# Kernel optimization log

Hardware: AMD Instinct MI355X
Metric: run time of the kernel (lower is better)

Reference implementation:

```python
import jax, jax.numpy as jnp
import numpy as np
from jax import lax

B, S, H, I, E, TOP_K = 4, 4096, 2048, 1024, 8, 2


def setup_inputs() -> dict:
    key = jax.random.key(0)
    k1, k2, k3, k4, k5 = jax.random.split(key, 5)
    scale = 0.02  # realistic init scale so router logits are well-conditioned
    return {
        "x": jax.random.normal(k1, (B, S, H), dtype=jnp.float32),
        "gate_w": jax.random.normal(k2, (E, H), dtype=jnp.float32) * scale,
        "wg": jax.random.normal(k3, (E, H, I), dtype=jnp.float32) * scale,
        "wu": jax.random.normal(k4, (E, H, I), dtype=jnp.float32) * scale,
        "wd": jax.random.normal(k5, (E, I, H), dtype=jnp.float32) * scale,
    }


def reference(x, gate_w, wg, wu, wd):
    b, s, h = x.shape
    xt = x.reshape(b * s, h)                      # [T, H]
    router_logits = xt @ gate_w.T                 # [T, E]
    probs = jax.nn.softmax(router_logits, axis=-1)
    topk_w, topk_idx = lax.top_k(probs, TOP_K)    # [T, K]
    T = xt.shape[0]
    # combine[t, e] = routing weight of expert e for token t (0 if not in top-k)
    combine = jnp.zeros((T, E), xt.dtype).at[
        jnp.arange(T)[:, None], topk_idx
    ].set(topk_w)

    # scan over experts; each step is one grouped SwiGLU MLP over all tokens,
    # weighted by the (mostly-zero) combine column -> identical math to the
    # torch gather/index_add dispatch.
    def step(acc, ew):
        wgi, wui, wdi, c = ew                     # [H,I],[H,I],[I,H],[T]
        hdn = jax.nn.silu(xt @ wgi) * (xt @ wui)  # [T, I]
        return acc + c[:, None] * (hdn @ wdi), None

    acc, _ = lax.scan(step, jnp.zeros_like(xt), (wg, wu, wd, combine.T))
    return acc.reshape(b, s, h), router_logits
```

## Files before the change

kernel.cpp:

```cpp
#include <hip/hip_runtime.h>

#define T_TOK 16384
#define H_DIM 2048
#define I_DIM 1024
#define E_NUM 8

static const size_t F_WGT = 0;
static const size_t F_WUT = 33554432ull;
static const size_t F_XH  = 67108864ull;
static const size_t F_Y2  = 0;
static const size_t F_WDT = 134217728ull;
static const size_t F_HDN = 167772160ull;
static const size_t F_TOK = 234881024ull;
static const size_t F_WT  = 235405312ull;
static const size_t F_IDX = 235929600ull;
static const size_t F_CNT = 236060672ull;

typedef float f32x4 __attribute__((ext_vector_type(4)));
typedef _Float16 f16x8 __attribute__((ext_vector_type(8)));
typedef _Float16 f16x4 __attribute__((ext_vector_type(4)));

__device__ __forceinline__ void gload_lds16(const void* g, void* l) {
  __builtin_amdgcn_global_load_lds(
      (const __attribute__((address_space(1))) unsigned int*)g,
      (__attribute__((address_space(3))) unsigned int*)l, 16, 0, 0);
}

__global__ __launch_bounds__(256) void wconv_kernel(
    const float* __restrict__ wg, const float* __restrict__ wu,
    const float* __restrict__ wd, _Float16* __restrict__ wgT,
    _Float16* __restrict__ wuT, _Float16* __restrict__ wdT) {
  const int bx = blockIdx.x;
  const int w = bx >> 12;
  const int r2 = bx & 4095;
  const int e = r2 >> 9;
  const int t = r2 & 511;

  const float* src;
  _Float16* dst;
  int R, C;
  if (w == 0)      { src = wg; dst = wgT; R = H_DIM; C = I_DIM; }
  else if (w == 1) { src = wu; dst = wuT; R = H_DIM; C = I_DIM; }
  else             { src = wd; dst = wdT; R = I_DIM; C = H_DIM; }
  src += (size_t)e * R * C;
  dst += (size_t)e * R * C;

  const int tiles_c = C >> 6;
  const int tr = t / tiles_c;
  const int tc = t % tiles_c;

  __shared__ float tile[64][65];
  const int tid = threadIdx.x;

#pragma unroll
  for (int c = 0; c < 4; ++c) {
    const int q = c * 256 + tid;
    const int row = q >> 4;
    const int col4 = (q & 15) * 4;
    const float4 v = *(const float4*)(src + (size_t)(tr * 64 + row) * C + tc * 64 + col4);
    tile[row][col4 + 0] = v.x;
    tile[row][col4 + 1] = v.y;
    tile[row][col4 + 2] = v.z;
    tile[row][col4 + 3] = v.w;
  }
  __syncthreads();
#pragma unroll
  for (int c = 0; c < 4; ++c) {
    const int q = c * 256 + tid;
    const int row = q >> 4;
    const int col4 = (q & 15) * 4;
    f16x4 o = { (_Float16)tile[col4 + 0][row], (_Float16)tile[col4 + 1][row],
                (_Float16)tile[col4 + 2][row], (_Float16)tile[col4 + 3][row] };
    *(f16x4*)(dst + (size_t)(tc * 64 + row) * R + tr * 64 + col4) = o;
  }
}

__global__ __launch_bounds__(256) void router_kernel(
    const float* __restrict__ x, const float* __restrict__ gw,
    float* __restrict__ logits, int* __restrict__ tok_list,
    float* __restrict__ wt_list, int* __restrict__ idx2,
    int* __restrict__ counts, _Float16* __restrict__ xh) {
  const int lane = threadIdx.x & 63;
  const int wave = threadIdx.x >> 6;
  const int t = blockIdx.x * 4 + wave;
  const float* xr = x + (size_t)t * H_DIM;

  float xv[32];
#pragma unroll
  for (int j = 0; j < 32; ++j) xv[j] = xr[lane + j * 64];

  _Float16* xhr = xh + (size_t)t * H_DIM;
#pragma unroll
  for (int j = 0; j < 32; ++j) xhr[lane + j * 64] = (_Float16)xv[j];

  float lg[E_NUM];
#pragma unroll
  for (int e = 0; e < E_NUM; ++e) {
    const float* gr = gw + e * H_DIM;
    float s = 0.f;
#pragma unroll
    for (int j = 0; j < 32; ++j) s += xv[j] * gr[lane + j * 64];
#pragma unroll
    for (int off = 32; off > 0; off >>= 1) s += __shfl_xor(s, off, 64);
    lg[e] = s;
  }

  if (lane == 0) {
#pragma unroll
    for (int e = 0; e < E_NUM; ++e) logits[(size_t)t * E_NUM + e] = lg[e];
    float mx = lg[0];
#pragma unroll
    for (int e = 1; e < E_NUM; ++e) mx = fmaxf(mx, lg[e]);
    float se = 0.f;
#pragma unroll
    for (int e = 0; e < E_NUM; ++e) se += expf(lg[e] - mx);
    int i1 = 0; float b1 = lg[0];
#pragma unroll
    for (int e = 1; e < E_NUM; ++e) { if (lg[e] > b1) { b1 = lg[e]; i1 = e; } }
    int i2 = -1; float b2 = -1e30f;
#pragma unroll
    for (int e = 0; e < E_NUM; ++e) { if (e != i1 && lg[e] > b2) { b2 = lg[e]; i2 = e; } }
    const float p1 = expf(b1 - mx) / se;
    const float p2 = expf(b2 - mx) / se;
    int pos = atomicAdd(&counts[i1], 1);
    tok_list[i1 * T_TOK + pos] = t;
    wt_list[i1 * T_TOK + pos] = p1;
    idx2[t * 2] = (i1 << 16) | pos;
    pos = atomicAdd(&counts[i2], 1);
    tok_list[i2 * T_TOK + pos] = t;
    wt_list[i2 * T_TOK + pos] = p2;
    idx2[t * 2 + 1] = (i2 << 16) | pos;
  }
}

__global__ __launch_bounds__(256) void gemm1_kernel(
    const _Float16* __restrict__ xh, const _Float16* __restrict__ wgT,
    const _Float16* __restrict__ wuT, const int* __restrict__ tok_list,
    const int* __restrict__ counts, _Float16* __restrict__ hdn) {
  const int cpx = (E_NUM * 128 * 8) >> 3;
  int bx = blockIdx.x;
  bx = (bx & 7) * cpx + (bx >> 3);

  const int cb = bx & 7;
  const int rb = (bx >> 3) & 127;
  const int e = bx >> 10;
  const int n_e = counts[e];
  const int row0 = rb * 128;
  if (row0 >= n_e) return;
  int goff = 0;
#pragma unroll
  for (int j = 0; j < E_NUM; ++j) goff += (j < e) ? counts[j] : 0;
  const int rem = min(128, n_e - row0);

  __shared__ int toks[128];
  __shared__ __attribute__((aligned(16))) _Float16 As[2][128 * 32];
  __shared__ __attribute__((aligned(16))) _Float16 Bg[2][128 * 32];
  __shared__ __attribute__((aligned(16))) _Float16 Bu[2][128 * 32];

  const int tid = threadIdx.x;
  if (tid < 128) {
    int idx = row0 + tid;
    if (idx > n_e - 1) idx = n_e - 1;
    toks[tid] = tok_list[e * T_TOK + idx];
  }
  __syncthreads();

  const int lane = tid & 63;
  const int wid = tid >> 6;
  const int wr = (wid >> 1) * 64;
  const int wcl = (wid & 1) * 64;
  const int n0 = cb * 128;

  const _Float16* wgTe = wgT + ((size_t)e * I_DIM + n0) * H_DIM;
  const _Float16* wuTe = wuT + ((size_t)e * I_DIM + n0) * H_DIM;

  const _Float16* asrc[2];
  int bofs[2], dofs[2];
#pragma unroll
  for (int c = 0; c < 2; ++c) {
    const int q = c * 256 + tid;
    const int rr = q >> 2;
    const int ch = q & 3;
    const int sch = ch ^ ((rr >> 1) & 3);
    asrc[c] = xh + (size_t)toks[rr] * H_DIM + sch * 8;
    bofs[c] = rr * H_DIM + sch * 8;
    dofs[c] = q * 8;
  }

  const f32x4 z4 = {0.f, 0.f, 0.f, 0.f};
  f32x4 accg[4][4], accu[4][4];
#pragma unroll
  for (int m = 0; m < 4; ++m)
#pragma unroll
    for (int n = 0; n < 4; ++n) { accg[m][n] = z4; accu[m][n] = z4; }

  const int cl = lane & 15;
  const int kq = lane >> 4;

  int aoff[4], boffr[4];
#pragma unroll
  for (int m = 0; m < 4; ++m) {
    const int row = wr + m * 16 + cl;
    aoff[m] = row * 32 + ((kq ^ ((row >> 1) & 3)) * 8);
  }
#pragma unroll
  for (int n = 0; n < 4; ++n) {
    const int row = wcl + n * 16 + cl;
    boffr[n] = row * 32 + ((kq ^ ((row >> 1) & 3)) * 8);
  }

#pragma unroll
  for (int c = 0; c < 2; ++c) {
    gload_lds16(asrc[c], &As[0][0] + dofs[c]);
    gload_lds16(wgTe + bofs[c], &Bg[0][0] + dofs[c]);
    gload_lds16(wuTe + bofs[c], &Bu[0][0] + dofs[c]);
  }
  asm volatile("s_waitcnt vmcnt(0)" ::: "memory");
  __builtin_amdgcn_s_barrier();
  __builtin_amdgcn_sched_barrier(0);

  const int NK = H_DIM / 32;
  for (int t = 0; t < NK; ++t) {
    const int cur = t & 1;
    if (t + 1 < NK) {
      const int kn = (t + 1) * 32;
#pragma unroll
      for (int c = 0; c < 2; ++c) {
        gload_lds16(asrc[c] + kn, &As[cur ^ 1][0] + dofs[c]);
        gload_lds16(wgTe + bofs[c] + kn, &Bg[cur ^ 1][0] + dofs[c]);
        gload_lds16(wuTe + bofs[c] + kn, &Bu[cur ^ 1][0] + dofs[c]);
      }
    }
    const _Float16* Ac = &As[cur][0];
    const _Float16* Gc = &Bg[cur][0];
    const _Float16* Uc = &Bu[cur][0];
    f16x8 af[4], bg[4], bu[4];
#pragma unroll
    for (int m = 0; m < 4; ++m) af[m] = *(const f16x8*)(Ac + aoff[m]);
#pragma unroll
    for (int n = 0; n < 4; ++n) {
      bg[n] = *(const f16x8*)(Gc + boffr[n]);
      bu[n] = *(const f16x8*)(Uc + boffr[n]);
    }
#pragma unroll
    for (int m = 0; m < 4; ++m)
#pragma unroll
      for (int n = 0; n < 4; ++n) {
        accg[m][n] = __builtin_amdgcn_mfma_f32_16x16x32_f16(af[m], bg[n], accg[m][n], 0, 0, 0);
        accu[m][n] = __builtin_amdgcn_mfma_f32_16x16x32_f16(af[m], bu[n], accu[m][n], 0, 0, 0);
      }
    asm volatile("s_waitcnt vmcnt(0)" ::: "memory");
    __builtin_amdgcn_s_barrier();
    __builtin_amdgcn_sched_barrier(0);
  }

  const int rq = lane >> 4;
#pragma unroll
  for (int m = 0; m < 4; ++m) {
#pragma unroll
    for (int r = 0; r < 4; ++r) {
      const int row = wr + m * 16 + rq * 4 + r;
      if (row < rem) {
        const size_t grow = (size_t)(goff + row0 + row);
#pragma unroll
        for (int n = 0; n < 4; ++n) {
          const float g = accg[m][n][r];
          const float u = accu[m][n][r];
          const float h = g / (1.f + __expf(-g)) * u;
          hdn[grow * I_DIM + n0 + wcl + n * 16 + cl] = (_Float16)h;
        }
      }
    }
  }
}

__global__ __launch_bounds__(256) void gemm2_kernel(
    const _Float16* __restrict__ hdn, const _Float16* __restrict__ wdT,
    const int* __restrict__ tok_list, const float* __restrict__ wt_list,
    const int* __restrict__ counts, _Float16* __restrict__ y2) {
  const int cpx = (E_NUM * 128 * 16) >> 3;
  int bx = blockIdx.x;
  bx = (bx & 7) * cpx + (bx >> 3);

  const int nb = bx & 15;
  const int rb = (bx >> 4) & 127;
  const int e = bx >> 11;
  const int n_e = counts[e];
  const int row0 = rb * 128;
  if (row0 >= n_e) return;
  int goff = 0;
#pragma unroll
  for (int j = 0; j < E_NUM; ++j) goff += (j < e) ? counts[j] : 0;
  const int rem = min(128, n_e - row0);

  __shared__ float wts[128];
  __shared__ __attribute__((aligned(16))) _Float16 As[2][128 * 32];
  __shared__ __attribute__((aligned(16))) _Float16 Bs[2][128 * 32];

  const int tid = threadIdx.x;
  if (tid < 128) {
    int idx = row0 + tid;
    const bool valid = (idx < n_e);
    wts[tid] = valid ? wt_list[e * T_TOK + min(idx, n_e - 1)] : 0.f;
  }
  __syncthreads();

  const int lane = tid & 63;
  const int wid = tid >> 6;
  const int wr = (wid >> 1) * 64;
  const int wcl = (wid & 1) * 64;
  const int h0 = nb * 128;

  const _Float16* wdTe = wdT + ((size_t)e * H_DIM + h0) * I_DIM;
  const _Float16* hdnb = hdn + (size_t)(goff + row0) * I_DIM;

  const _Float16* asrc[2];
  int bofs[2], dofs[2];
#pragma unroll
  for (int c = 0; c < 2; ++c) {
    const int q = c * 256 + tid;
    const int rr = q >> 2;
    const int ch = q & 3;
    const int sch = ch ^ ((rr >> 1) & 3);
    const int rrc = min(rr, rem - 1);
    asrc[c] = hdnb + (size_t)rrc * I_DIM + sch * 8;
    bofs[c] = rr * I_DIM + sch * 8;
    dofs[c] = q * 8;
  }

  const f32x4 z4 = {0.f, 0.f, 0.f, 0.f};
  f32x4 acc[4][4];
#pragma unroll
  for (int m = 0; m < 4; ++m)
#pragma unroll
    for (int n = 0; n < 4; ++n) acc[m][n] = z4;

  const int cl = lane & 15;
  const int kq = lane >> 4;

  int aoff[4], boffr[4];
#pragma unroll
  for (int m = 0; m < 4; ++m) {
    const int row = wr + m * 16 + cl;
    aoff[m] = row * 32 + ((kq ^ ((row >> 1) & 3)) * 8);
  }
#pragma unroll
  for (int n = 0; n < 4; ++n) {
    const int row = wcl + n * 16 + cl;
    boffr[n] = row * 32 + ((kq ^ ((row >> 1) & 3)) * 8);
  }

#pragma unroll
  for (int c = 0; c < 2; ++c) {
    gload_lds16(asrc[c], &As[0][0] + dofs[c]);
    gload_lds16(wdTe + bofs[c], &Bs[0][0] + dofs[c]);
  }
  asm volatile("s_waitcnt vmcnt(0)" ::: "memory");
  __builtin_amdgcn_s_barrier();
  __builtin_amdgcn_sched_barrier(0);

  const int NK = I_DIM / 32;
  for (int t = 0; t < NK; ++t) {
    const int cur = t & 1;
    if (t + 1 < NK) {
      const int kn = (t + 1) * 32;
#pragma unroll
      for (int c = 0; c < 2; ++c) {
        gload_lds16(asrc[c] + kn, &As[cur ^ 1][0] + dofs[c]);
        gload_lds16(wdTe + bofs[c] + kn, &Bs[cur ^ 1][0] + dofs[c]);
      }
    }
    const _Float16* Ac = &As[cur][0];
    const _Float16* Bc = &Bs[cur][0];
    f16x8 af[4], bf[4];
#pragma unroll
    for (int m = 0; m < 4; ++m) af[m] = *(const f16x8*)(Ac + aoff[m]);
#pragma unroll
    for (int n = 0; n < 4; ++n) bf[n] = *(const f16x8*)(Bc + boffr[n]);
#pragma unroll
    for (int m = 0; m < 4; ++m)
#pragma unroll
      for (int n = 0; n < 4; ++n)
        acc[m][n] = __builtin_amdgcn_mfma_f32_16x16x32_f16(af[m], bf[n], acc[m][n], 0, 0, 0);
    asm volatile("s_waitcnt vmcnt(0)" ::: "memory");
    __builtin_amdgcn_s_barrier();
    __builtin_amdgcn_sched_barrier(0);
  }

  const int rq = lane >> 4;
#pragma unroll
  for (int m = 0; m < 4; ++m) {
#pragma unroll
    for (int r = 0; r < 4; ++r) {
      const int row = wr + m * 16 + rq * 4 + r;
      if (row < rem) {
        const float w = wts[row];
        _Float16* yrow = y2 + (size_t)(goff + row0 + row) * H_DIM + h0 + wcl;
#pragma unroll
        for (int n = 0; n < 4; ++n)
          yrow[n * 16 + cl] = (_Float16)(acc[m][n][r] * w);
      }
    }
  }
}

__global__ __launch_bounds__(256) void combine_kernel(
    const _Float16* __restrict__ y2, const int* __restrict__ idx2,
    const int* __restrict__ counts, float* __restrict__ out) {
  const int t = blockIdx.x;
  int pref[E_NUM];
  int run = 0;
#pragma unroll
  for (int e = 0; e < E_NUM; ++e) { pref[e] = run; run += counts[e]; }
  const int p0 = idx2[t * 2];
  const int p1 = idx2[t * 2 + 1];
  const size_t r0 = (size_t)(pref[p0 >> 16] + (p0 & 0xFFFF)) * H_DIM;
  const size_t r1 = (size_t)(pref[p1 >> 16] + (p1 & 0xFFFF)) * H_DIM;
  const int o = threadIdx.x * 8;
  const f16x8 a = *(const f16x8*)(y2 + r0 + o);
  const f16x8 b = *(const f16x8*)(y2 + r1 + o);
  float* orow = out + (size_t)t * H_DIM + o;
  float4 lo = { (float)a[0] + (float)b[0], (float)a[1] + (float)b[1],
                (float)a[2] + (float)b[2], (float)a[3] + (float)b[3] };
  float4 hi = { (float)a[4] + (float)b[4], (float)a[5] + (float)b[5],
                (float)a[6] + (float)b[6], (float)a[7] + (float)b[7] };
  *(float4*)orow = lo;
  *(float4*)(orow + 4) = hi;
}

extern "C" void kernel_launch(void* const* d_in, const int* in_sizes, int n_in,
                              void* d_out, int out_size, void* d_ws, size_t ws_size,
                              hipStream_t stream) {
  (void)in_sizes; (void)n_in; (void)out_size; (void)ws_size;
  const float* x      = (const float*)d_in[0];
  const float* gate_w = (const float*)d_in[1];
  const float* wg     = (const float*)d_in[2];
  const float* wu     = (const float*)d_in[3];
  const float* wd     = (const float*)d_in[4];
  float* out0 = (float*)d_out;
  float* out1 = out0 + (size_t)T_TOK * H_DIM;

  char* ws = (char*)d_ws;
  _Float16* wgT = (_Float16*)(ws + F_WGT);
  _Float16* wuT = (_Float16*)(ws + F_WUT);
  _Float16* xh  = (_Float16*)(ws + F_XH);
  _Float16* y2  = (_Float16*)(ws + F_Y2);
  _Float16* wdT = (_Float16*)(ws + F_WDT);
  _Float16* hdn = (_Float16*)(ws + F_HDN);
  int* tok_list = (int*)(ws + F_TOK);
  float* wt_list = (float*)(ws + F_WT);
  int* idx2 = (int*)(ws + F_IDX);
  int* counts = (int*)(ws + F_CNT);

  hipMemsetAsync(counts, 0, 64, stream);
  wconv_kernel<<<12288, 256, 0, stream>>>(wg, wu, wd, wgT, wuT, wdT);
  router_kernel<<<T_TOK / 4, 256, 0, stream>>>(x, gate_w, out1, tok_list, wt_list, idx2, counts, xh);
  gemm1_kernel<<<E_NUM * 128 * 8, 256, 0, stream>>>(xh, wgT, wuT, tok_list, counts, hdn);
  gemm2_kernel<<<E_NUM * 128 * 16, 256, 0, stream>>>(hdn, wdT, tok_list, wt_list, counts, y2);
  combine_kernel<<<T_TOK, 256, 0, stream>>>(y2, idx2, counts, out0);
}
```

Measured before the change: 1.391 ms.

## Widen gemm2 N-tile to 256 and interleave gate/up loads in gemm1

gemm2 now computes a 128x256 output tile per block, with each wave covering 64x128 and 32 accumulators, and launches half as many blocks. This reuses each hdn A tile across twice as many columns and halves A traffic. gemm1 splits the gate and up MFMA phases and issues the up-weight prefetch between them, and both kernels raise wave priority around the MFMA bursts with s_setprio. The larger accumulator set in gemm2 raises register pressure and may lower occupancy.

```diff
diff --git a/kernel.cpp b/kernel.cpp
--- a/kernel.cpp
+++ b/kernel.cpp
@@ -222,33 +222,44 @@
   const int NK = H_DIM / 32;
   for (int t = 0; t < NK; ++t) {
     const int cur = t & 1;
+    const _Float16* Ac = &As[cur][0];
+    const _Float16* Gc = &Bg[cur][0];
+    const _Float16* Uc = &Bu[cur][0];
     if (t + 1 < NK) {
       const int kn = (t + 1) * 32;
 #pragma unroll
       for (int c = 0; c < 2; ++c) {
         gload_lds16(asrc[c] + kn, &As[cur ^ 1][0] + dofs[c]);
         gload_lds16(wgTe + bofs[c] + kn, &Bg[cur ^ 1][0] + dofs[c]);
-        gload_lds16(wuTe + bofs[c] + kn, &Bu[cur ^ 1][0] + dofs[c]);
       }
     }
-    const _Float16* Ac = &As[cur][0];
-    const _Float16* Gc = &Bg[cur][0];
-    const _Float16* Uc = &Bu[cur][0];
     f16x8 af[4], bg[4], bu[4];
 #pragma unroll
     for (int m = 0; m < 4; ++m) af[m] = *(const f16x8*)(Ac + aoff[m]);
 #pragma unroll
-    for (int n = 0; n < 4; ++n) {
-      bg[n] = *(const f16x8*)(Gc + boffr[n]);
-      bu[n] = *(const f16x8*)(Uc + boffr[n]);
+    for (int n = 0; n < 4; ++n) bg[n] = *(const f16x8*)(Gc + boffr[n]);
+    __builtin_amdgcn_s_setprio(1);
+#pragma unroll
+    for (int m = 0; m < 4; ++m)
+#pragma unroll
+      for (int n = 0; n < 4; ++n)
+        accg[m][n] = __builtin_amdgcn_mfma_f32_16x16x32_f16(af[m], bg[n], accg[m][n], 0, 0, 0);
+    __builtin_amdgcn_s_setprio(0);
+    if (t + 1 < NK) {
+      const int kn = (t + 1) * 32;
+#pragma unroll
+      for (int c = 0; c < 2; ++c)
+        gload_lds16(wuTe + bofs[c] + kn, &Bu[cur ^ 1][0] + dofs[c]);
     }
 #pragma unroll
+    for (int n = 0; n < 4; ++n) bu[n] = *(const f16x8*)(Uc + boffr[n]);
+    __builtin_amdgcn_s_setprio(1);
+#pragma unroll
     for (int m = 0; m < 4; ++m)
 #pragma unroll
-      for (int n = 0; n < 4; ++n) {
-        accg[m][n] = __builtin_amdgcn_mfma_f32_16x16x32_f16(af[m], bg[n], accg[m][n], 0, 0, 0);
+      for (int n = 0; n < 4; ++n)
         accu[m][n] = __builtin_amdgcn_mfma_f32_16x16x32_f16(af[m], bu[n], accu[m][n], 0, 0, 0);
-      }
+    __builtin_amdgcn_s_setprio(0);
     asm volatile("s_waitcnt vmcnt(0)" ::: "memory");
     __builtin_amdgcn_s_barrier();
     __builtin_amdgcn_sched_barrier(0);
@@ -278,13 +289,13 @@
     const _Float16* __restrict__ hdn, const _Float16* __restrict__ wdT,
     const int* __restrict__ tok_list, const float* __restrict__ wt_list,
     const int* __restrict__ counts, _Float16* __restrict__ y2) {
-  const int cpx = (E_NUM * 128 * 16) >> 3;
+  const int cpx = (E_NUM * 128 * 8) >> 3;
   int bx = blockIdx.x;
   bx = (bx & 7) * cpx + (bx >> 3);
 
-  const int nb = bx & 15;
-  const int rb = (bx >> 4) & 127;
-  const int e = bx >> 11;
+  const int nb = bx & 7;
+  const int rb = (bx >> 3) & 127;
+  const int e = bx >> 10;
   const int n_e = counts[e];
   const int row0 = rb * 128;
   if (row0 >= n_e) return;
@@ -295,7 +306,7 @@
 
   __shared__ float wts[128];
   __shared__ __attribute__((aligned(16))) _Float16 As[2][128 * 32];
-  __shared__ __attribute__((aligned(16))) _Float16 Bs[2][128 * 32];
+  __shared__ __attribute__((aligned(16))) _Float16 Bs[2][256 * 32];
 
   const int tid = threadIdx.x;
   if (tid < 128) {
@@ -308,14 +319,14 @@
   const int lane = tid & 63;
   const int wid = tid >> 6;
   const int wr = (wid >> 1) * 64;
-  const int wcl = (wid & 1) * 64;
-  const int h0 = nb * 128;
+  const int wcl = (wid & 1) * 128;
+  const int h0 = nb * 256;
 
   const _Float16* wdTe = wdT + ((size_t)e * H_DIM + h0) * I_DIM;
   const _Float16* hdnb = hdn + (size_t)(goff + row0) * I_DIM;
 
   const _Float16* asrc[2];
-  int bofs[2], dofs[2];
+  int adofs[2];
 #pragma unroll
   for (int c = 0; c < 2; ++c) {
     const int q = c * 256 + tid;
@@ -324,37 +335,45 @@
     const int sch = ch ^ ((rr >> 1) & 3);
     const int rrc = min(rr, rem - 1);
     asrc[c] = hdnb + (size_t)rrc * I_DIM + sch * 8;
+    adofs[c] = q * 8;
+  }
+  int bofs[4], bdofs[4];
+#pragma unroll
+  for (int c = 0; c < 4; ++c) {
+    const int q = c * 256 + tid;
+    const int rr = q >> 2;
+    const int ch = q & 3;
+    const int sch = ch ^ ((rr >> 1) & 3);
     bofs[c] = rr * I_DIM + sch * 8;
-    dofs[c] = q * 8;
+    bdofs[c] = q * 8;
   }
 
   const f32x4 z4 = {0.f, 0.f, 0.f, 0.f};
-  f32x4 acc[4][4];
+  f32x4 acc[4][8];
 #pragma unroll
   for (int m = 0; m < 4; ++m)
 #pragma unroll
-    for (int n = 0; n < 4; ++n) acc[m][n] = z4;
+    for (int n = 0; n < 8; ++n) acc[m][n] = z4;
 
   const int cl = lane & 15;
   const int kq = lane >> 4;
 
-  int aoff[4], boffr[4];
+  int aoff[4], boffr[8];
 #pragma unroll
   for (int m = 0; m < 4; ++m) {
     const int row = wr + m * 16 + cl;
     aoff[m] = row * 32 + ((kq ^ ((row >> 1) & 3)) * 8);
   }
 #pragma unroll
-  for (int n = 0; n < 4; ++n) {
+  for (int n = 0; n < 8; ++n) {
     const int row = wcl + n * 16 + cl;
     boffr[n] = row * 32 + ((kq ^ ((row >> 1) & 3)) * 8);
   }
 
 #pragma unroll
-  for (int c = 0; c < 2; ++c) {
-    gload_lds16(asrc[c], &As[0][0] + dofs[c]);
-    gload_lds16(wdTe + bofs[c], &Bs[0][0] + dofs[c]);
-  }
+  for (int c = 0; c < 2; ++c) gload_lds16(asrc[c], &As[0][0] + adofs[c]);
+#pragma unroll
+  for (int c = 0; c < 4; ++c) gload_lds16(wdTe + bofs[c], &Bs[0][0] + bdofs[c]);
   asm volatile("s_waitcnt vmcnt(0)" ::: "memory");
   __builtin_amdgcn_s_barrier();
   __builtin_amdgcn_sched_barrier(0);
@@ -365,23 +384,24 @@
     if (t + 1 < NK) {
       const int kn = (t + 1) * 32;
 #pragma unroll
-      for (int c = 0; c < 2; ++c) {
-        gload_lds16(asrc[c] + kn, &As[cur ^ 1][0] + dofs[c]);
-        gload_lds16(wdTe + bofs[c] + kn, &Bs[cur ^ 1][0] + dofs[c]);
-      }
+      for (int c = 0; c < 2; ++c) gload_lds16(asrc[c] + kn, &As[cur ^ 1][0] + adofs[c]);
+#pragma unroll
+      for (int c = 0; c < 4; ++c) gload_lds16(wdTe + bofs[c] + kn, &Bs[cur ^ 1][0] + bdofs[c]);
     }
     const _Float16* Ac = &As[cur][0];
     const _Float16* Bc = &Bs[cur][0];
-    f16x8 af[4], bf[4];
+    f16x8 af[4], bf[8];
 #pragma unroll
     for (int m = 0; m < 4; ++m) af[m] = *(const f16x8*)(Ac + aoff[m]);
 #pragma unroll
-    for (int n = 0; n < 4; ++n) bf[n] = *(const f16x8*)(Bc + boffr[n]);
+    for (int n = 0; n < 8; ++n) bf[n] = *(const f16x8*)(Bc + boffr[n]);
+    __builtin_amdgcn_s_setprio(1);
 #pragma unroll
     for (int m = 0; m < 4; ++m)
 #pragma unroll
-      for (int n = 0; n < 4; ++n)
+      for (int n = 0; n < 8; ++n)
         acc[m][n] = __builtin_amdgcn_mfma_f32_16x16x32_f16(af[m], bf[n], acc[m][n], 0, 0, 0);
+    __builtin_amdgcn_s_setprio(0);
     asm volatile("s_waitcnt vmcnt(0)" ::: "memory");
     __builtin_amdgcn_s_barrier();
     __builtin_amdgcn_sched_barrier(0);
@@ -397,7 +417,7 @@
         const float w = wts[row];
         _Float16* yrow = y2 + (size_t)(goff + row0 + row) * H_DIM + h0 + wcl;
 #pragma unroll
-        for (int n = 0; n < 4; ++n)
+        for (int n = 0; n < 8; ++n)
           yrow[n * 16 + cl] = (_Float16)(acc[m][n][r] * w);
       }
     }
@@ -456,6 +476,6 @@
   wconv_kernel<<<12288, 256, 0, stream>>>(wg, wu, wd, wgT, wuT, wdT);
   router_kernel<<<T_TOK / 4, 256, 0, stream>>>(x, gate_w, out1, tok_list, wt_list, idx2, counts, xh);
   gemm1_kernel<<<E_NUM * 128 * 8, 256, 0, stream>>>(xh, wgT, wuT, tok_list, counts, hdn);
-  gemm2_kernel<<<E_NUM * 128 * 16, 256, 0, stream>>>(hdn, wdT, tok_list, wt_list, counts, y2);
+  gemm2_kernel<<<E_NUM * 128 * 8, 256, 0, stream>>>(hdn, wdT, tok_list, wt_list, counts, y2);
   combine_kernel<<<T_TOK, 256, 0, stream>>>(y2, idx2, counts, out0);
 }
```

Result: slower. 1.456 ms (+4.7%).
